# Kernel tuning notes

Hardware: AMD Instinct MI355X
Metric: run time of the kernel (lower is better)

Reference implementation:

```python
import jax, jax.numpy as jnp
import numpy as np

N = 100000      # num nodes
E = 1000000     # num edges
R = 50          # num relations
B = 2           # num bases (hard-coded in source)
IN, HID, OUT = 128, 64, 64


def setup_inputs() -> dict:
    key = jax.random.key(0)
    ks = jax.random.split(key, 12)
    def xavier(k, shape):
        fan_in, fan_out = shape[-2], shape[-1]
        lim = (6.0 / (fan_in + fan_out)) ** 0.5
        return jax.random.uniform(k, shape, jnp.float32, -lim, lim)
    return {
        "node_emb": xavier(ks[0], (N, IN)),
        "basis1": xavier(ks[1], (B, IN, HID)),
        "comp1": xavier(ks[2], (R, B)),
        "loop_w1": xavier(ks[3], (IN, HID)),
        "bias1": jnp.zeros((HID,), jnp.float32),
        "basis2": xavier(ks[4], (B, HID, OUT)),
        "comp2": xavier(ks[5], (R, B)),
        "loop_w2": xavier(ks[6], (HID, OUT)),
        "bias2": jnp.zeros((OUT,), jnp.float32),
        "src": jax.random.randint(ks[7], (E,), 0, N, jnp.int32),
        "dst": jax.random.randint(ks[8], (E,), 0, N, jnp.int32),
        "etypes": jax.random.randint(ks[9], (E,), 0, R, jnp.int32),
    }


def _rel_graph_conv(h, basis, comp, loop_w, bias, src, dst, etypes, act):
    # Basis-decomposed R-GCN layer (DGL RelGraphConv, regularizer='basis'):
    #   W_r = sum_b comp[r,b] * basis[b];  m_e = W_{etype_e} h_{src_e}
    # Low-rank form: project with each basis first (2 dense GEMMs), then mix
    # per-edge with the relation coefficients, then scatter-add by dst.
    hb = jnp.einsum('nd,bdo->nbo', h, basis)          # [N, B, out]
    c = comp[etypes]                                   # [E, B]
    msg = jnp.einsum('eb,ebo->eo', c, hb[src])         # gather [E,B,out] -> [E,out]
    agg = jax.ops.segment_sum(msg, dst, num_segments=h.shape[0])  # scatter-add
    return act(agg + h @ loop_w + bias)                # self-loop + bias + activation


def reference(node_emb, basis1, comp1, loop_w1, bias1,
              basis2, comp2, loop_w2, bias2, src, dst, etypes):
    h = _rel_graph_conv(node_emb, basis1, comp1, loop_w1, bias1,
                        src, dst, etypes, jnp.tanh)
    out = _rel_graph_conv(h, basis2, comp2, loop_w2, bias2,
                          src, dst, etypes, jax.nn.relu)
    return out
```

## Files before the change

kernel.cpp:

```cpp
#include <hip/hip_runtime.h>
#include <math.h>


typedef short          short8 __attribute__((ext_vector_type(8)));
typedef float          f32x4  __attribute__((ext_vector_type(4)));
typedef unsigned short u16;

#define NCHUNK 256

static __device__ __forceinline__ u16 bf16_rne(float x) {
    unsigned u = __float_as_uint(x);
    return (u16)((u + 0x7fffu + ((u >> 16) & 1u)) >> 16);
}
static __device__ __forceinline__ float bf16_f32(u16 h) {
    return __uint_as_float(((unsigned)h) << 16);
}

__device__ __forceinline__ void wconv_body(
    int tid,
    const float* __restrict__ loopw1, const float* __restrict__ basis1,
    const float* __restrict__ loopw2, const float* __restrict__ basis2,
    u16* __restrict__ wt1h, u16* __restrict__ wt1l,
    u16* __restrict__ wt2h, u16* __restrict__ wt2l)
{
    if (tid < 192 * 128) {
        const int j = tid >> 7, k = tid & 127;
        const float w = (j < 64)
            ? loopw1[k * 64 + j]
            : basis1[(size_t)((j - 64) >> 6) * (128 * 64) + k * 64 + ((j - 64) & 63)];
        const u16 h = bf16_rne(w);
        wt1h[tid] = h;
        wt1l[tid] = bf16_rne(w - bf16_f32(h));
    }
    if (tid < 192 * 64) {
        const int j = tid >> 6, k = tid & 63;
        const float w = (j < 64)
            ? loopw2[k * 64 + j]
            : basis2[(size_t)((j - 64) >> 6) * (64 * 64) + k * 64 + ((j - 64) & 63)];
        const u16 h = bf16_rne(w);
        wt2h[tid] = h;
        wt2l[tid] = bf16_rne(w - bf16_f32(h));
    }
}

__global__ __launch_bounds__(256) void prep_count(
    const int* __restrict__ dst, int* __restrict__ cnt, int nE, int nB,
    const float* __restrict__ loopw1, const float* __restrict__ basis1,
    const float* __restrict__ loopw2, const float* __restrict__ basis2,
    u16* __restrict__ wt1h, u16* __restrict__ wt1l,
    u16* __restrict__ wt2h, u16* __restrict__ wt2l)
{
    const int t = threadIdx.x;
    if (blockIdx.x >= NCHUNK) {
        wconv_body((blockIdx.x - NCHUNK) * 256 + t,
                   loopw1, basis1, loopw2, basis2, wt1h, wt1l, wt2h, wt2l);
        return;
    }
    __shared__ int lh[1024];
    for (int b = t; b < 1024; b += 256) lh[b] = 0;
    __syncthreads();
    const int chunk = (nE + NCHUNK - 1) / NCHUNK;
    const int e0 = blockIdx.x * chunk;
    const int e1 = min(nE, e0 + chunk);
    for (int e = e0 + t; e < e1; e += 256)
        atomicAdd(&lh[dst[e] >> 7], 1);
    __syncthreads();
    for (int b = t; b < nB; b += 256)
        cnt[blockIdx.x * nB + b] = lh[b];
}

template<int K>
__global__ __launch_bounds__(256, 4) void rgcn_dense_mfma(
    const float* __restrict__ x,
    const u16* __restrict__ wth,
    const u16* __restrict__ wtl,
    const float* __restrict__ bias,
    float* __restrict__ self,
    unsigned* __restrict__ hbb,
    int nNodes)
{
    constexpr int KC  = K / 32;
    constexpr int GW  = K / 8;
    constexpr int GMW = GW - 1;
    __shared__ u16 wlds[48 * 2 * K];

    const int n0   = blockIdx.x * 64;
    const int lane = threadIdx.x & 63;
    const int w    = threadIdx.x >> 6;
    const int rl   = lane & 15;
    const int kb   = lane >> 4;

    const int row = n0 + w * 16 + rl;
    short8 Ah[KC], Al[KC];
    #pragma unroll
    for (int kc = 0; kc < KC; ++kc) {
        float v[8];
        if (row < nNodes) {
            const float* xp = x + (size_t)row * K + kc * 32 + kb * 8;
            const float4 a = *reinterpret_cast<const float4*>(xp);
            const float4 b = *reinterpret_cast<const float4*>(xp + 4);
            v[0] = a.x; v[1] = a.y; v[2] = a.z; v[3] = a.w;
            v[4] = b.x; v[5] = b.y; v[6] = b.z; v[7] = b.w;
        } else {
            #pragma unroll
            for (int i = 0; i < 8; ++i) v[i] = 0.f;
        }
        #pragma unroll
        for (int i = 0; i < 8; ++i) {
            const u16 h = bf16_rne(v[i]);
            Ah[kc][i] = (short)h;
            Al[kc][i] = (short)bf16_rne(v[i] - bf16_f32(h));
        }
    }

    f32x4 acc[12];
    #pragma unroll
    for (int j = 0; j < 12; ++j) acc[j] = (f32x4){0.f, 0.f, 0.f, 0.f};

    #pragma unroll
    for (int cc = 0; cc < 4; ++cc) {
        if (cc) __syncthreads();
        for (int gi = threadIdx.x; gi < 48 * 2 * GW; gi += 256) {
            const int ch = gi / (2 * GW);
            const int r2 = gi - ch * 2 * GW;
            const int s  = r2 / GW;
            const int g  = r2 - s * GW;
            const u16* sp = (s == 0 ? wth : wtl)
                          + (size_t)(cc * 48 + ch) * K + g * 8;
            const short8 vv = *reinterpret_cast<const short8*>(sp);
            *reinterpret_cast<short8*>(
                &wlds[((ch * 2 + s) * GW + (g ^ (ch & GMW))) * 8]) = vv;
        }
        __syncthreads();

        #pragma unroll
        for (int j16h = 0; j16h < 3; ++j16h) {
            const int ch = j16h * 16 + rl;
            const u16* bbase = &wlds[(ch * 2) * GW * 8];
            #pragma unroll
            for (int kc = 0; kc < KC; ++kc) {
                const int gp = (kc * 4 + kb) ^ (ch & GMW);
                const short8 Bh =
                    *reinterpret_cast<const short8*>(bbase + gp * 8);
                const short8 Bl =
                    *reinterpret_cast<const short8*>(bbase + (GW + gp) * 8);
                f32x4 a = acc[cc * 3 + j16h];
                a = __builtin_amdgcn_mfma_f32_16x16x32_bf16(Ah[kc], Bh, a, 0, 0, 0);
                a = __builtin_amdgcn_mfma_f32_16x16x32_bf16(Ah[kc], Bl, a, 0, 0, 0);
                a = __builtin_amdgcn_mfma_f32_16x16x32_bf16(Al[kc], Bh, a, 0, 0, 0);
                acc[cc * 3 + j16h] = a;
            }
        }
    }

    const int rowbase = n0 + w * 16 + kb * 4;
    #pragma unroll
    for (int j16 = 0; j16 < 4; ++j16) {
        const float bj = bias[j16 * 16 + rl];
        #pragma unroll
        for (int r = 0; r < 4; ++r) {
            const int rr = rowbase + r;
            if (rr < nNodes)
                self[(size_t)rr * 64 + j16 * 16 + rl] = acc[j16][r] + bj;
        }
    }
    #pragma unroll
    for (int j16 = 4; j16 < 8; ++j16) {
        #pragma unroll
        for (int r = 0; r < 4; ++r) {
            const int rr = rowbase + r;
            if (rr < nNodes)
                hbb[(size_t)rr * 64 + (j16 - 4) * 16 + rl] =
                    (unsigned)bf16_rne(acc[j16][r])
                  | ((unsigned)bf16_rne(acc[j16 + 4][r]) << 16);
        }
    }
}

__global__ __launch_bounds__(NCHUNK) void bkt_chunkscan(
    int* __restrict__ cnt, int* __restrict__ tot, int nB)
{
    __shared__ int sm[NCHUNK];
    const int b = blockIdx.x, t = threadIdx.x;
    const int v = cnt[t * nB + b];
    sm[t] = v;
    __syncthreads();
    for (int off = 1; off < NCHUNK; off <<= 1) {
        const int u = (t >= off) ? sm[t - off] : 0;
        __syncthreads();
        sm[t] += u;
        __syncthreads();
    }
    cnt[t * nB + b] = sm[t] - v;
    if (t == NCHUNK - 1) tot[b] = sm[t];
}

__global__ __launch_bounds__(1024) void bkt_boff(
    const int* __restrict__ tot, int* __restrict__ boff, int nB, int nE)
{
    __shared__ int sm[1024];
    const int t = threadIdx.x;
    const int v = (t < nB) ? tot[t] : 0;
    sm[t] = v; __syncthreads();
    for (int off = 1; off < 1024; off <<= 1) {
        const int u = (t >= off) ? sm[t - off] : 0;
        __syncthreads();
        sm[t] += u;
        __syncthreads();
    }
    if (t < nB) boff[t] = sm[t] - v;
    if (t == 0) boff[nB] = nE;
}

__global__ __launch_bounds__(256) void bkt_scatter(
    const int* __restrict__ src, const int* __restrict__ dst,
    const int* __restrict__ et, const int* __restrict__ cnt,
    const int* __restrict__ boff, unsigned* __restrict__ rec,
    int nE, int nB)
{
    __shared__ int lcur[1024];
    const int t = threadIdx.x;
    const int c = blockIdx.x;
    for (int b = t; b < nB; b += 256)
        lcur[b] = boff[b] + cnt[c * nB + b];
    __syncthreads();
    const int chunk = (nE + NCHUNK - 1) / NCHUNK;
    const int e0 = c * chunk;
    const int e1 = min(nE, e0 + chunk);
    for (int e = e0 + t; e < e1; e += 256) {
        const int d = dst[e];
        const int p = atomicAdd(&lcur[d >> 7], 1);
        rec[p] = ((unsigned)(d & 127) << 23)
               | ((unsigned)src[e] << 6)
               | (unsigned)et[e];
    }
}

__global__ __launch_bounds__(256) void bkt_sort(
    const unsigned* __restrict__ rec, unsigned* __restrict__ rec2,
    const int* __restrict__ boff, int* __restrict__ rowptr,
    int nNodes)
{
    __shared__ int cnt[128];
    __shared__ int pos[128];
    const int b = blockIdx.x;
    const int t = threadIdx.x;
    const int beg = boff[b], end = boff[b + 1];
    if (t < 128) cnt[t] = 0;
    __syncthreads();
    for (int i = beg + t; i < end; i += 256)
        atomicAdd(&cnt[rec[i] >> 23], 1);
    __syncthreads();
    if (t < 128) pos[t] = cnt[t];
    __syncthreads();
    for (int off = 1; off < 128; off <<= 1) {
        int u = 0;
        if (t < 128 && t >= off) u = pos[t - off];
        __syncthreads();
        if (t < 128) pos[t] += u;
        __syncthreads();
    }
    if (t < 128) {
        const int ex = beg + pos[t] - cnt[t];
        pos[t] = ex;
        const int n = (b << 7) + t;
        if (n < nNodes) rowptr[n] = ex;
    }
    __syncthreads();
    for (int i = beg + t; i < end; i += 256) {
        const unsigned r = rec[i];
        const int p = atomicAdd(&pos[r >> 23], 1);
        rec2[p] = r;
    }
}

template<int ACT>
__global__ __launch_bounds__(256) void rgcn_agg(
    const unsigned* __restrict__ hbb,
    const float* __restrict__ comp,
    const int* __restrict__ rowptr,
    const unsigned* __restrict__ rec2,
    float* __restrict__ io,
    int nNodes, int nEdges)
{
    const int lane = threadIdx.x & 63;
    const int w  = (blockIdx.x * 256 + threadIdx.x) >> 6;
    const int nW = (gridDim.x * 256) >> 6;
    const float2* __restrict__ comp2 = reinterpret_cast<const float2*>(comp);
    for (int n = w; n < nNodes; n += nW) {
        const int beg = rowptr[n];
        const int end = (n == nNodes - 1) ? nEdges : rowptr[n + 1];
        const float self = io[(size_t)n * 64 + lane];
        float acc0 = 0.f, acc1 = 0.f;
        for (int base = beg; base < end; base += 64) {
            const int cnt = min(64, end - base);
            const unsigned r = (lane < cnt) ? rec2[base + lane] : 0u;
            for (int i = 0; i < cnt; i += 16) {
                unsigned v[16]; int tt[16];
                #pragma unroll
                for (int k = 0; k < 16; ++k) {
                    const unsigned rk =
                        (unsigned)__builtin_amdgcn_readlane((int)r, i + k);
                    tt[k] = (int)(rk & 63u);
                    v[k] = hbb[(size_t)((rk >> 6) & 0x1FFFFu) * 64 + lane];
                }
                #pragma unroll
                for (int k = 0; k < 16; ++k) {
                    if (i + k < cnt) {
                        const float2 c = comp2[tt[k]];
                        acc0 = fmaf(c.x, __uint_as_float(v[k] << 16), acc0);
                        acc1 = fmaf(c.y, __uint_as_float(v[k] & 0xffff0000u), acc1);
                    }
                }
            }
        }
        float o = self + acc0 + acc1;
        o = (ACT == 0) ? tanhf(o) : fmaxf(o, 0.f);
        io[(size_t)n * 64 + lane] = o;
    }
}

extern "C" void kernel_launch(void* const* d_in, const int* in_sizes, int n_in,
                              void* d_out, int out_size, void* d_ws, size_t ws_size,
                              hipStream_t stream)
{
    const float* node_emb = (const float*)d_in[0];
    const float* basis1   = (const float*)d_in[1];
    const float* comp1    = (const float*)d_in[2];
    const float* loop_w1  = (const float*)d_in[3];
    const float* bias1    = (const float*)d_in[4];
    const float* basis2   = (const float*)d_in[5];
    const float* comp2    = (const float*)d_in[6];
    const float* loop_w2  = (const float*)d_in[7];
    const float* bias2    = (const float*)d_in[8];
    const int*   src      = (const int*)d_in[9];
    const int*   dst      = (const int*)d_in[10];
    const int*   et       = (const int*)d_in[11];

    const int N = in_sizes[0] / 128;
    const int E = in_sizes[9];
    const int nB = (N + 127) / 128;

    float* out = (float*)d_out;

    unsigned* hbb    = (unsigned*)d_ws;
    float*    h      = (float*)(hbb + (size_t)N * 64);
    unsigned* rec    = (unsigned*)(h + (size_t)N * 64);
    unsigned* rec2   = rec + E;
    int*      cnt    = (int*)(rec2 + E);
    int*      tot    = cnt + NCHUNK * nB;
    int*      boff   = tot + nB;
    int*      rowptr = boff + nB + 1;
    u16*      wt1h   = (u16*)(rowptr + N);
    u16*      wt1l   = wt1h + 192 * 128;
    u16*      wt2h   = wt1l + 192 * 128;
    u16*      wt2l   = wt2h + 192 * 64;

    const int nBlkDense = (N + 63) / 64;
    const int nBlkAgg   = (N + 3) / 4;

    prep_count<<<NCHUNK + 96, 256, 0, stream>>>(
        dst, cnt, E, nB, loop_w1, basis1, loop_w2, basis2,
        wt1h, wt1l, wt2h, wt2l);

    bkt_chunkscan<<<nB, NCHUNK, 0, stream>>>(cnt, tot, nB);
    bkt_boff     <<<1,    1024, 0, stream>>>(tot, boff, nB, E);
    bkt_scatter  <<<NCHUNK, 256, 0, stream>>>(src, dst, et, cnt, boff, rec, E, nB);
    bkt_sort     <<<nB,     256, 0, stream>>>(rec, rec2, boff, rowptr, N);

    rgcn_dense_mfma<128><<<nBlkDense, 256, 0, stream>>>(
        node_emb, wt1h, wt1l, bias1, h, hbb, N);
    rgcn_agg<0><<<nBlkAgg, 256, 0, stream>>>(
        hbb, comp1, rowptr, rec2, h, N, E);

    rgcn_dense_mfma<64><<<nBlkDense, 256, 0, stream>>>(
        h, wt2h, wt2l, bias2, out, hbb, N);
    rgcn_agg<1><<<nBlkAgg, 256, 0, stream>>>(
        hbb, comp2, rowptr, rec2, out, N, E);
}
```

Baseline: 200.5 us.

## Double-buffer dense weight tiles, enlarge dense blocks, use bf16 dot2 in aggregation

The dense MFMA kernel now runs 512-thread blocks covering 128 rows. For K=128 it double-buffers the weight chunks in LDS, prefetching the next chunk into registers while the current one computes; for K=64 it loads all 192 columns at once. The aggregation kernel packs the relation coefficients as bf16 pairs and uses v_dot2_f32_bf16 inline asm, with smaller 8-edge batches and remainder loops, replacing the two scalar FMAs and the per-edge bounds checks. Rounding the coefficients to bf16 adds some precision error, and the larger blocks and LDS footprint may reduce occupancy.

```diff
diff --git a/kernel.cpp b/kernel.cpp
--- a/kernel.cpp
+++ b/kernel.cpp
@@ -15,13 +15,18 @@
 static __device__ __forceinline__ float bf16_f32(u16 h) {
     return __uint_as_float(((unsigned)h) << 16);
 }
+
+#define DOT2_ACC(acc, vv, cc) \
+    asm("v_dot2_f32_bf16 %0, %1, %2, %0" : "+v"(acc) : "v"(vv), "s"(cc))
 
 __device__ __forceinline__ void wconv_body(
     int tid,
     const float* __restrict__ loopw1, const float* __restrict__ basis1,
     const float* __restrict__ loopw2, const float* __restrict__ basis2,
+    const float* __restrict__ comp1, const float* __restrict__ comp2,
     u16* __restrict__ wt1h, u16* __restrict__ wt1l,
-    u16* __restrict__ wt2h, u16* __restrict__ wt2l)
+    u16* __restrict__ wt2h, u16* __restrict__ wt2l,
+    unsigned* __restrict__ cpk1, unsigned* __restrict__ cpk2)
 {
     if (tid < 192 * 128) {
         const int j = tid >> 7, k = tid & 127;
@@ -41,19 +46,28 @@
         wt2h[tid] = h;
         wt2l[tid] = bf16_rne(w - bf16_f32(h));
     }
+    if (tid < 50) {
+        cpk1[tid] = (unsigned)bf16_rne(comp1[2 * tid])
+                  | ((unsigned)bf16_rne(comp1[2 * tid + 1]) << 16);
+        cpk2[tid] = (unsigned)bf16_rne(comp2[2 * tid])
+                  | ((unsigned)bf16_rne(comp2[2 * tid + 1]) << 16);
+    }
 }
 
 __global__ __launch_bounds__(256) void prep_count(
     const int* __restrict__ dst, int* __restrict__ cnt, int nE, int nB,
     const float* __restrict__ loopw1, const float* __restrict__ basis1,
     const float* __restrict__ loopw2, const float* __restrict__ basis2,
+    const float* __restrict__ comp1, const float* __restrict__ comp2,
     u16* __restrict__ wt1h, u16* __restrict__ wt1l,
-    u16* __restrict__ wt2h, u16* __restrict__ wt2l)
+    u16* __restrict__ wt2h, u16* __restrict__ wt2l,
+    unsigned* __restrict__ cpk1, unsigned* __restrict__ cpk2)
 {
     const int t = threadIdx.x;
     if (blockIdx.x >= NCHUNK) {
         wconv_body((blockIdx.x - NCHUNK) * 256 + t,
-                   loopw1, basis1, loopw2, basis2, wt1h, wt1l, wt2h, wt2l);
+                   loopw1, basis1, loopw2, basis2, comp1, comp2,
+                   wt1h, wt1l, wt2h, wt2l, cpk1, cpk2);
         return;
     }
     __shared__ int lh[1024];
@@ -70,7 +84,7 @@
 }
 
 template<int K>
-__global__ __launch_bounds__(256, 4) void rgcn_dense_mfma(
+__global__ __launch_bounds__(512, 2) void rgcn_dense_mfma(
     const float* __restrict__ x,
     const u16* __restrict__ wth,
     const u16* __restrict__ wtl,
@@ -79,12 +93,18 @@
     unsigned* __restrict__ hbb,
     int nNodes)
 {
-    constexpr int KC  = K / 32;
-    constexpr int GW  = K / 8;
-    constexpr int GMW = GW - 1;
-    __shared__ u16 wlds[48 * 2 * K];
-
-    const int n0   = blockIdx.x * 64;
+    constexpr int KC    = K / 32;
+    constexpr int GW    = K / 8;
+    constexpr int GMW   = GW - 1;
+    constexpr int CCOLS = (K == 128) ? 48 : 192;
+    constexpr int NCH   = 192 / CCOLS;
+    constexpr int JH    = CCOLS / 16;
+    constexpr int TG    = CCOLS * 2 * GW;
+    constexpr int PG    = TG / 512;
+    constexpr int BUF   = CCOLS * 2 * K;
+    __shared__ u16 wlds[24576];
+
+    const int n0   = blockIdx.x * 128;
     const int lane = threadIdx.x & 63;
     const int w    = threadIdx.x >> 6;
     const int rl   = lane & 15;
@@ -117,26 +137,35 @@
     #pragma unroll
     for (int j = 0; j < 12; ++j) acc[j] = (f32x4){0.f, 0.f, 0.f, 0.f};
 
-    #pragma unroll
-    for (int cc = 0; cc < 4; ++cc) {
-        if (cc) __syncthreads();
-        for (int gi = threadIdx.x; gi < 48 * 2 * GW; gi += 256) {
+    auto load_chunk = [&](int cc, short8* sreg) {
+        #pragma unroll
+        for (int i = 0; i < PG; ++i) {
+            const int gi = (int)threadIdx.x + i * 512;
             const int ch = gi / (2 * GW);
             const int r2 = gi - ch * 2 * GW;
             const int s  = r2 / GW;
             const int g  = r2 - s * GW;
-            const u16* sp = (s == 0 ? wth : wtl)
-                          + (size_t)(cc * 48 + ch) * K + g * 8;
-            const short8 vv = *reinterpret_cast<const short8*>(sp);
+            sreg[i] = *reinterpret_cast<const short8*>(
+                (s == 0 ? wth : wtl) + (size_t)(cc * CCOLS + ch) * K + g * 8);
+        }
+    };
+    auto write_chunk = [&](u16* buf, const short8* sreg) {
+        #pragma unroll
+        for (int i = 0; i < PG; ++i) {
+            const int gi = (int)threadIdx.x + i * 512;
+            const int ch = gi / (2 * GW);
+            const int r2 = gi - ch * 2 * GW;
+            const int s  = r2 / GW;
+            const int g  = r2 - s * GW;
             *reinterpret_cast<short8*>(
-                &wlds[((ch * 2 + s) * GW + (g ^ (ch & GMW))) * 8]) = vv;
-        }
-        __syncthreads();
-
-        #pragma unroll
-        for (int j16h = 0; j16h < 3; ++j16h) {
+                &buf[((ch * 2 + s) * GW + (g ^ (ch & GMW))) * 8]) = sreg[i];
+        }
+    };
+    auto compute = [&](int cc, const u16* buf) {
+        #pragma unroll
+        for (int j16h = 0; j16h < JH; ++j16h) {
             const int ch = j16h * 16 + rl;
-            const u16* bbase = &wlds[(ch * 2) * GW * 8];
+            const u16* bbase = &buf[(ch * 2) * GW * 8];
             #pragma unroll
             for (int kc = 0; kc < KC; ++kc) {
                 const int gp = (kc * 4 + kb) ^ (ch & GMW);
@@ -144,11 +173,35 @@
                     *reinterpret_cast<const short8*>(bbase + gp * 8);
                 const short8 Bl =
                     *reinterpret_cast<const short8*>(bbase + (GW + gp) * 8);
-                f32x4 a = acc[cc * 3 + j16h];
+                f32x4 a = acc[cc * JH + j16h];
                 a = __builtin_amdgcn_mfma_f32_16x16x32_bf16(Ah[kc], Bh, a, 0, 0, 0);
                 a = __builtin_amdgcn_mfma_f32_16x16x32_bf16(Ah[kc], Bl, a, 0, 0, 0);
                 a = __builtin_amdgcn_mfma_f32_16x16x32_bf16(Al[kc], Bh, a, 0, 0, 0);
-                acc[cc * 3 + j16h] = a;
+                acc[cc * JH + j16h] = a;
+            }
+        }
+    };
+
+    if constexpr (NCH == 1) {
+        short8 s0[PG];
+        load_chunk(0, s0);
+        write_chunk(wlds, s0);
+        __syncthreads();
+        compute(0, wlds);
+    } else {
+        short8 s0[PG];
+        load_chunk(0, s0);
+        write_chunk(wlds, s0);
+        __syncthreads();
+        #pragma unroll
+        for (int cc = 0; cc < 4; ++cc) {
+            short8 sn[PG];
+            if (cc < 3) load_chunk(cc + 1, sn);
+            compute(cc, &wlds[(cc & 1) * BUF]);
+            __syncthreads();
+            if (cc < 3) {
+                write_chunk(&wlds[((cc + 1) & 1) * BUF], sn);
+                __syncthreads();
             }
         }
     }
@@ -277,7 +330,7 @@
 template<int ACT>
 __global__ __launch_bounds__(256) void rgcn_agg(
     const unsigned* __restrict__ hbb,
-    const float* __restrict__ comp,
+    const unsigned* __restrict__ cpk,
     const int* __restrict__ rowptr,
     const unsigned* __restrict__ rec2,
     float* __restrict__ io,
@@ -286,7 +339,6 @@
     const int lane = threadIdx.x & 63;
     const int w  = (blockIdx.x * 256 + threadIdx.x) >> 6;
     const int nW = (gridDim.x * 256) >> 6;
-    const float2* __restrict__ comp2 = reinterpret_cast<const float2*>(comp);
     for (int n = w; n < nNodes; n += nW) {
         const int beg = rowptr[n];
         const int end = (n == nNodes - 1) ? nEdges : rowptr[n + 1];
@@ -295,23 +347,43 @@
         for (int base = beg; base < end; base += 64) {
             const int cnt = min(64, end - base);
             const unsigned r = (lane < cnt) ? rec2[base + lane] : 0u;
-            for (int i = 0; i < cnt; i += 16) {
-                unsigned v[16]; int tt[16];
+            int i = 0;
+            for (; i + 8 <= cnt; i += 8) {
+                int ss[8]; unsigned cp[8];
                 #pragma unroll
-                for (int k = 0; k < 16; ++k) {
+                for (int k = 0; k < 8; ++k) {
                     const unsigned rk =
                         (unsigned)__builtin_amdgcn_readlane((int)r, i + k);
-                    tt[k] = (int)(rk & 63u);
-                    v[k] = hbb[(size_t)((rk >> 6) & 0x1FFFFu) * 64 + lane];
+                    ss[k] = (int)((rk >> 6) & 0x1FFFFu);
+                    cp[k] = cpk[rk & 63u];
                 }
+                unsigned v[8];
                 #pragma unroll
-                for (int k = 0; k < 16; ++k) {
-                    if (i + k < cnt) {
-                        const float2 c = comp2[tt[k]];
-                        acc0 = fmaf(c.x, __uint_as_float(v[k] << 16), acc0);
-                        acc1 = fmaf(c.y, __uint_as_float(v[k] & 0xffff0000u), acc1);
-                    }
+                for (int k = 0; k < 8; ++k)
+                    v[k] = hbb[(size_t)ss[k] * 64 + lane];
+                #pragma unroll
+                for (int k = 0; k < 8; ++k) {
+                    if (k & 1) { DOT2_ACC(acc1, v[k], cp[k]); }
+                    else       { DOT2_ACC(acc0, v[k], cp[k]); }
                 }
+            }
+            for (; i + 2 <= cnt; i += 2) {
+                const unsigned rA =
+                    (unsigned)__builtin_amdgcn_readlane((int)r, i);
+                const unsigned rB =
+                    (unsigned)__builtin_amdgcn_readlane((int)r, i + 1);
+                const unsigned cA = cpk[rA & 63u], cB = cpk[rB & 63u];
+                const unsigned vA = hbb[(size_t)((rA >> 6) & 0x1FFFFu) * 64 + lane];
+                const unsigned vB = hbb[(size_t)((rB >> 6) & 0x1FFFFu) * 64 + lane];
+                DOT2_ACC(acc0, vA, cA);
+                DOT2_ACC(acc1, vB, cB);
+            }
+            if (i < cnt) {
+                const unsigned rA =
+                    (unsigned)__builtin_amdgcn_readlane((int)r, i);
+                const unsigned cA = cpk[rA & 63u];
+                const unsigned vA = hbb[(size_t)((rA >> 6) & 0x1FFFFu) * 64 + lane];
+                DOT2_ACC(acc0, vA, cA);
             }
         }
         float o = self + acc0 + acc1;
@@ -355,26 +427,28 @@
     u16*      wt1l   = wt1h + 192 * 128;
     u16*      wt2h   = wt1l + 192 * 128;
     u16*      wt2l   = wt2h + 192 * 64;
-
-    const int nBlkDense = (N + 63) / 64;
+    unsigned* cpk1   = (unsigned*)(wt2l + 192 * 64);
+    unsigned* cpk2   = cpk1 + 64;
+
+    const int nBlkDense = (N + 127) / 128;
     const int nBlkAgg   = (N + 3) / 4;
 
     prep_count<<<NCHUNK + 96, 256, 0, stream>>>(
-        dst, cnt, E, nB, loop_w1, basis1, loop_w2, basis2,
-        wt1h, wt1l, wt2h, wt2l);
+        dst, cnt, E, nB, loop_w1, basis1, loop_w2, basis2, comp1, comp2,
+        wt1h, wt1l, wt2h, wt2l, cpk1, cpk2);
 
     bkt_chunkscan<<<nB, NCHUNK, 0, stream>>>(cnt, tot, nB);
     bkt_boff     <<<1,    1024, 0, stream>>>(tot, boff, nB, E);
     bkt_scatter  <<<NCHUNK, 256, 0, stream>>>(src, dst, et, cnt, boff, rec, E, nB);
     bkt_sort     <<<nB,     256, 0, stream>>>(rec, rec2, boff, rowptr, N);
 
-    rgcn_dense_mfma<128><<<nBlkDense, 256, 0, stream>>>(
+    rgcn_dense_mfma<128><<<nBlkDense, 512, 0, stream>>>(
         node_emb, wt1h, wt1l, bias1, h, hbb, N);
     rgcn_agg<0><<<nBlkAgg, 256, 0, stream>>>(
-        hbb, comp1, rowptr, rec2, h, N, E);
-
-    rgcn_dense_mfma<64><<<nBlkDense, 256, 0, stream>>>(
+        hbb, cpk1, rowptr, rec2, h, N, E);
+
+    rgcn_dense_mfma<64><<<nBlkDense, 512, 0, stream>>>(
         h, wt2h, wt2l, bias2, out, hbb, N);
     rgcn_agg<1><<<nBlkAgg, 256, 0, stream>>>(
-        hbb, comp2, rowptr, rec2, out, N, E);
-}
+        hbb, cpk2, rowptr, rec2, out, N, E);
+}
```

After: 191.0 us. 1.05x faster.
